# Kernel optimization log

Hardware: AMD Instinct MI355X
Metric: run time of the kernel (lower is better)

Reference implementation:

```python
import jax, jax.numpy as jnp
import numpy as np

K_SIZE = 3
SIGMA = 1.3


def _gauss_kernel():
    # Matches the original: K[y,x] = exp(-(x^2+y^2)/(2*sigma^2)), then normalized to sum 1.
    pad = K_SIZE // 2
    coords = jnp.arange(-pad, pad + 1, dtype=jnp.float32)
    g = jnp.exp(-(coords[:, None] ** 2 + coords[None, :] ** 2) / (2.0 * SIGMA ** 2))
    return g / g.sum()


def setup_inputs() -> dict:
    key = jax.random.key(0)
    im = jax.random.uniform(key, (1, 4096, 4096, 3), dtype=jnp.float32)  # non-negative photon-count-like image
    return {"im": im}


def reference(im):
    x = jnp.squeeze(im, 0)                       # [H, W, C]
    # Anscombe transform
    at = 2.0 * jnp.sqrt(x + 0.375)
    # 3x3 depthwise Gaussian blur with zero padding (pad=1), per channel
    C = at.shape[-1]
    kern = jnp.broadcast_to(_gauss_kernel()[:, :, None, None], (K_SIZE, K_SIZE, 1, C))
    y = jax.lax.conv_general_dilated(
        at[None], kern, window_strides=(1, 1), padding="SAME",
        dimension_numbers=("NHWC", "HWIO", "NHWC"), feature_group_count=C)[0]
    y = jnp.clip(y, 0.0, 255.0)
    # Inverse Anscombe transform (unbiased closed-form approximation)
    s = jnp.sqrt(jnp.float32(1.5))
    out = 0.25 * y ** 2 + 0.25 * s / y - (11.0 / 8.0) / (y ** 2) + 0.625 * s / (y ** 3) - 0.125
    return out
```

## Files before the change

### kernel.cpp

```cpp
#include <hip/hip_runtime.h>
#include <cmath>

constexpr int H   = 4096;
constexpr int W   = 4096;
constexpr int C   = 3;
constexpr int WF  = W * C;
constexpr int EPT = 8;
constexpr int TW  = 256 * EPT;
constexpr int RPT = 16;

typedef float f32x4 __attribute__((ext_vector_type(4)));

__device__ __forceinline__ float ans1(float v) {
    return 2.0f * __builtin_amdgcn_sqrtf(v + 0.375f);
}
__device__ __forceinline__ float4 ans4(float4 v) {
    return make_float4(ans1(v.x), ans1(v.y), ans1(v.z), ans1(v.w));
}

__global__ __launch_bounds__(256, 4) void anscombe_gauss_kernel(
    const float* __restrict__ in, float* __restrict__ out,
    float wa, float wb, float c1, float c3)
{
    const int tid = threadIdx.x;
    const int gc  = blockIdx.x * TW + tid * EPT;
    const int h0  = blockIdx.y * RPT;

    const bool okL = (gc >= 4);
    const bool okR = (gc + 12 <= WF);
    const int offL = okL ? gc - 4 : gc;
    const int offR = okR ? gc + 8 : gc;

    const float4 cfill = make_float4(-0.375f, -0.375f, -0.375f, -0.375f);

    auto loadrow = [&](int h, float4& lo, float4& hi, float4& hl, float4& hr) {
        if ((unsigned)h < (unsigned)H) {
            const float* rp = in + (long)h * WF;
            lo = *(const float4*)(rp + gc);
            hi = *(const float4*)(rp + gc + 4);
            hl = *(const float4*)(rp + offL);
            hr = *(const float4*)(rp + offR);
            if (!okL) hl = cfill;
            if (!okR) hr = cfill;
        } else {
            lo = hi = hl = hr = cfill;
        }
    };

    float4 pl, ph, pL, pR;
    loadrow(h0 - 1, pl, ph, pL, pR);

    float hp[8] = {0,0,0,0,0,0,0,0};
    float hc[8] = {0,0,0,0,0,0,0,0};

    #pragma unroll
    for (int s = 0; s < RPT + 2; ++s) {
        const float4 vlo = pl, vhi = ph, vhl = pL, vhr = pR;
        if (s < RPT + 1) loadrow(h0 + s, pl, ph, pL, pR);

        const float4 alo = ans4(vlo), ahi = ans4(vhi);
        const float m3 = ans1(vhl.y), m2 = ans1(vhl.z), m1 = ans1(vhl.w);
        const float p8 = ans1(vhr.x), p9 = ans1(vhr.y), pA = ans1(vhr.z);

        const float e0 = alo.x, e1 = alo.y, e2 = alo.z, e3 = alo.w;
        const float e4 = ahi.x, e5 = ahi.y, e6 = ahi.z, e7 = ahi.w;

        float hn[8];
        hn[0] = wa * (m3 + e3) + wb * e0;
        hn[1] = wa * (m2 + e4) + wb * e1;
        hn[2] = wa * (m1 + e5) + wb * e2;
        hn[3] = wa * (e0 + e6) + wb * e3;
        hn[4] = wa * (e1 + e7) + wb * e4;
        hn[5] = wa * (e2 + p8) + wb * e5;
        hn[6] = wa * (e3 + p9) + wb * e6;
        hn[7] = wa * (e4 + pA) + wb * e7;

        if (s >= 2) {
            const int ho = h0 + s - 2;
            float o[8];
            #pragma unroll
            for (int j = 0; j < 8; ++j) {
                float y = wa * (hp[j] + hn[j]) + wb * hc[j];
                y = fminf(fmaxf(y, 0.0f), 255.0f);
                float ry = __builtin_amdgcn_rcpf(y);
                o[j] = fmaf(0.25f * y, y,
                        fmaf(ry, fmaf(ry, fmaf(ry, c3, -1.375f), c1), -0.125f));
            }
            float* op = out + (long)ho * WF + gc;
            f32x4 o0 = {o[0], o[1], o[2], o[3]};
            f32x4 o1 = {o[4], o[5], o[6], o[7]};
            __builtin_nontemporal_store(o0, (f32x4*)op);
            __builtin_nontemporal_store(o1, (f32x4*)(op + 4));
        }
        #pragma unroll
        for (int j = 0; j < 8; ++j) { hp[j] = hc[j]; hc[j] = hn[j]; }
    }
}

extern "C" void kernel_launch(void* const* d_in, const int* in_sizes, int n_in,
                              void* d_out, int out_size, void* d_ws, size_t ws_size,
                              hipStream_t stream) {
    const float* in = (const float*)d_in[0];
    float* out      = (float*)d_out;

    const double sig2x2 = 2.0 * 1.3 * 1.3;
    const double e1     = std::exp(-1.0 / sig2x2);
    const double inv1d  = 1.0 / (1.0 + 2.0 * e1);
    const float  wa     = (float)(e1 * inv1d);
    const float  wb     = (float)inv1d;

    const double s  = std::sqrt(1.5);
    const float  c1 = (float)(0.25  * s);
    const float  c3 = (float)(0.625 * s);

    dim3 grid(WF / TW, H / RPT);
    anscombe_gauss_kernel<<<grid, 256, 0, stream>>>(in, out, wa, wb, c1, c3);
}
```

Before: 84.53 us.

## Split each thread's columns into two coalesced halves and halve rows per block

Each thread now handles two float4 groups spaced half a tile apart instead of eight contiguous floats, so adjacent lanes touch adjacent 16-byte chunks for loads and stores. Each group loads its own left and right neighbour float4, giving six loads per row instead of four and recomputing the Anscombe transform on more halo elements. Rows per block drop from 16 to 8 and the occupancy hint rises to 8, which adds more vertical halo rows and more blocks in exchange for better coalescing and more waves in flight.

```diff
diff --git a/kernel.cpp b/kernel.cpp
--- a/kernel.cpp
+++ b/kernel.cpp
@@ -1,13 +1,13 @@
 #include <hip/hip_runtime.h>
 #include <cmath>
 
-constexpr int H   = 4096;
-constexpr int W   = 4096;
-constexpr int C   = 3;
-constexpr int WF  = W * C;
-constexpr int EPT = 8;
-constexpr int TW  = 256 * EPT;
-constexpr int RPT = 16;
+constexpr int H    = 4096;
+constexpr int W    = 4096;
+constexpr int C    = 3;
+constexpr int WF   = W * C;
+constexpr int TW   = 2048;
+constexpr int HALF = TW / 2;
+constexpr int RPT  = 8;
 
 typedef float f32x4 __attribute__((ext_vector_type(4)));
 
@@ -18,62 +18,63 @@
     return make_float4(ans1(v.x), ans1(v.y), ans1(v.z), ans1(v.w));
 }
 
-__global__ __launch_bounds__(256, 4) void anscombe_gauss_kernel(
+__global__ __launch_bounds__(256, 8) void anscombe_gauss_kernel(
     const float* __restrict__ in, float* __restrict__ out,
     float wa, float wb, float c1, float c3)
 {
     const int tid = threadIdx.x;
-    const int gc  = blockIdx.x * TW + tid * EPT;
+    const int p   = blockIdx.x * TW + tid * 4;
+    const int q   = p + HALF;
     const int h0  = blockIdx.y * RPT;
 
-    const bool okL = (gc >= 4);
-    const bool okR = (gc + 12 <= WF);
-    const int offL = okL ? gc - 4 : gc;
-    const int offR = okR ? gc + 8 : gc;
+    const bool okL0 = (p >= 4);
+    const bool okR1 = (q + 8 <= WF);
+    const int offL0 = okL0 ? p - 4 : p;
+    const int offR1 = okR1 ? q + 4 : q;
 
     const float4 cfill = make_float4(-0.375f, -0.375f, -0.375f, -0.375f);
 
-    auto loadrow = [&](int h, float4& lo, float4& hi, float4& hl, float4& hr) {
+    auto loadrow = [&](int h, float4& c0, float4& l0, float4& r0,
+                               float4& c1v, float4& l1, float4& r1) {
         if ((unsigned)h < (unsigned)H) {
             const float* rp = in + (long)h * WF;
-            lo = *(const float4*)(rp + gc);
-            hi = *(const float4*)(rp + gc + 4);
-            hl = *(const float4*)(rp + offL);
-            hr = *(const float4*)(rp + offR);
-            if (!okL) hl = cfill;
-            if (!okR) hr = cfill;
+            l0  = *(const float4*)(rp + offL0);
+            c0  = *(const float4*)(rp + p);
+            r0  = *(const float4*)(rp + p + 4);
+            l1  = *(const float4*)(rp + q - 4);
+            c1v = *(const float4*)(rp + q);
+            r1  = *(const float4*)(rp + offR1);
+            if (!okL0) l0 = cfill;
+            if (!okR1) r1 = cfill;
         } else {
-            lo = hi = hl = hr = cfill;
+            c0 = l0 = r0 = c1v = l1 = r1 = cfill;
         }
     };
 
-    float4 pl, ph, pL, pR;
-    loadrow(h0 - 1, pl, ph, pL, pR);
+    float4 pc0, pl0, pr0, pc1, pl1, pr1;
+    loadrow(h0 - 1, pc0, pl0, pr0, pc1, pl1, pr1);
 
     float hp[8] = {0,0,0,0,0,0,0,0};
     float hc[8] = {0,0,0,0,0,0,0,0};
 
     #pragma unroll
     for (int s = 0; s < RPT + 2; ++s) {
-        const float4 vlo = pl, vhi = ph, vhl = pL, vhr = pR;
-        if (s < RPT + 1) loadrow(h0 + s, pl, ph, pL, pR);
+        const float4 vc0 = pc0, vl0 = pl0, vr0 = pr0;
+        const float4 vc1 = pc1, vl1 = pl1, vr1 = pr1;
+        if (s < RPT + 1) loadrow(h0 + s, pc0, pl0, pr0, pc1, pl1, pr1);
 
-        const float4 alo = ans4(vlo), ahi = ans4(vhi);
-        const float m3 = ans1(vhl.y), m2 = ans1(vhl.z), m1 = ans1(vhl.w);
-        const float p8 = ans1(vhr.x), p9 = ans1(vhr.y), pA = ans1(vhr.z);
-
-        const float e0 = alo.x, e1 = alo.y, e2 = alo.z, e3 = alo.w;
-        const float e4 = ahi.x, e5 = ahi.y, e6 = ahi.z, e7 = ahi.w;
+        const float4 a0 = ans4(vc0), aL0 = ans4(vl0), aR0 = ans4(vr0);
+        const float4 a1 = ans4(vc1), aL1 = ans4(vl1), aR1 = ans4(vr1);
 
         float hn[8];
-        hn[0] = wa * (m3 + e3) + wb * e0;
-        hn[1] = wa * (m2 + e4) + wb * e1;
-        hn[2] = wa * (m1 + e5) + wb * e2;
-        hn[3] = wa * (e0 + e6) + wb * e3;
-        hn[4] = wa * (e1 + e7) + wb * e4;
-        hn[5] = wa * (e2 + p8) + wb * e5;
-        hn[6] = wa * (e3 + p9) + wb * e6;
-        hn[7] = wa * (e4 + pA) + wb * e7;
+        hn[0] = wa * (aL0.y + a0.w)  + wb * a0.x;
+        hn[1] = wa * (aL0.z + aR0.x) + wb * a0.y;
+        hn[2] = wa * (aL0.w + aR0.y) + wb * a0.z;
+        hn[3] = wa * (a0.x  + aR0.z) + wb * a0.w;
+        hn[4] = wa * (aL1.y + a1.w)  + wb * a1.x;
+        hn[5] = wa * (aL1.z + aR1.x) + wb * a1.y;
+        hn[6] = wa * (aL1.w + aR1.y) + wb * a1.z;
+        hn[7] = wa * (a1.x  + aR1.z) + wb * a1.w;
 
         if (s >= 2) {
             const int ho = h0 + s - 2;
@@ -86,11 +87,11 @@
                 o[j] = fmaf(0.25f * y, y,
                         fmaf(ry, fmaf(ry, fmaf(ry, c3, -1.375f), c1), -0.125f));
             }
-            float* op = out + (long)ho * WF + gc;
+            float* op = out + (long)ho * WF;
             f32x4 o0 = {o[0], o[1], o[2], o[3]};
             f32x4 o1 = {o[4], o[5], o[6], o[7]};
-            __builtin_nontemporal_store(o0, (f32x4*)op);
-            __builtin_nontemporal_store(o1, (f32x4*)(op + 4));
+            __builtin_nontemporal_store(o0, (f32x4*)(op + p));
+            __builtin_nontemporal_store(o1, (f32x4*)(op + q));
         }
         #pragma unroll
         for (int j = 0; j < 8; ++j) { hp[j] = hc[j]; hc[j] = hn[j]; }
```

Measured after the change: 289.7 us. 3.43x slower.
